# Performance work log

Hardware: AMD Instinct MI355X
Metric: run time of the kernel (lower is better)

## Reference

```python
import jax, jax.numpy as jnp
import numpy as np

H = 1024          # en_hidden_size
NUM_LAYERS = 3
NUM_CLASS = 60
IN_SIZE = 150
EPS = 1e-5


def _gru_dir(x, w_ih, w_hh, b_ih, b_hh):
    """Single-direction GRU run forward in time. x: [N,T,in] -> [N,T,H].
    PyTorch GRU cell math."""
    gi = jnp.einsum('nti,gi->ntg', x, w_ih) + b_ih  # [N,T,3H] input projections

    def step(h, gi_t):
        gh = h @ w_hh.T + b_hh
        i_r, i_z, i_n = jnp.split(gi_t, 3, axis=-1)
        h_r, h_z, h_n = jnp.split(gh, 3, axis=-1)
        r = jax.nn.sigmoid(i_r + h_r)
        z = jax.nn.sigmoid(i_z + h_z)
        n = jnp.tanh(i_n + r * h_n)
        h_new = (1.0 - z) * n + z * h
        return h_new, h_new

    h0 = jnp.zeros((x.shape[0], H), dtype=x.dtype)
    _, ys = jax.lax.scan(step, h0, jnp.swapaxes(gi, 0, 1))  # ys: [T,N,H]
    return jnp.swapaxes(ys, 0, 1)


def _bigru_forward(x, bn_gamma, bn_beta,
                   w_ih_0, w_hh_0, b_ih_0, b_hh_0,
                   w_ih_1, w_hh_1, b_ih_1, b_hh_1,
                   w_ih_2, w_hh_2, b_ih_2, b_hh_2,
                   fc_w, fc_b):
    # BatchNorm1d (train mode): stats over (N,T) per channel, biased variance.
    mean = jnp.mean(x, axis=(0, 1), keepdims=True)
    var = jnp.mean(jnp.square(x - mean), axis=(0, 1), keepdims=True)
    h_in = (x - mean) * jax.lax.rsqrt(var + EPS) * bn_gamma + bn_beta

    # NOTE: the original advances the bidirectional GRU one timestep at a time
    # while carrying the hidden state, so BOTH directions run forward in time.
    layer_params = [(w_ih_0, w_hh_0, b_ih_0, b_hh_0),
                    (w_ih_1, w_hh_1, b_ih_1, b_hh_1),
                    (w_ih_2, w_hh_2, b_ih_2, b_hh_2)]
    for (w_ih, w_hh, b_ih, b_hh) in layer_params:
        outs = [_gru_dir(h_in, w_ih[d], w_hh[d], b_ih[d], b_hh[d]) for d in range(2)]
        h_in = jnp.concatenate(outs, axis=-1)  # [N,T,2H]

    encoder_hidden = h_in                      # [N,T,2H]
    hidden = encoder_hidden[:, -1, :]          # seq_len == T for every sample
    out = hidden @ fc_w.T + fc_b               # [N, num_class]
    return out, encoder_hidden


def setup_inputs() -> dict:
    key = jax.random.key(0)
    ks = jax.random.split(key, 32)
    N, T = 256, 64
    s = 1.0 / np.sqrt(H)
    inp = {}
    inp['x'] = jax.random.normal(ks[0], (N, T, IN_SIZE), dtype=jnp.float32)
    inp['bn_gamma'] = jnp.ones((IN_SIZE,), jnp.float32)
    inp['bn_beta'] = jnp.zeros((IN_SIZE,), jnp.float32)
    in_sizes = [IN_SIZE, 2 * H, 2 * H]
    ki = 1
    for l in range(NUM_LAYERS):
        inp[f'w_ih_{l}'] = jax.random.uniform(ks[ki], (2, 3 * H, in_sizes[l]), jnp.float32, -s, s); ki += 1
        inp[f'w_hh_{l}'] = jax.random.uniform(ks[ki], (2, 3 * H, H), jnp.float32, -s, s); ki += 1
        inp[f'b_ih_{l}'] = jax.random.uniform(ks[ki], (2, 3 * H), jnp.float32, -s, s); ki += 1
        inp[f'b_hh_{l}'] = jax.random.uniform(ks[ki], (2, 3 * H), jnp.float32, -s, s); ki += 1
    inp['fc_w'] = jax.random.uniform(ks[ki], (NUM_CLASS, 2 * H), jnp.float32, -s, s); ki += 1
    inp['fc_b'] = jax.random.uniform(ks[ki], (NUM_CLASS,), jnp.float32, -s, s)
    return inp


def reference(x, bn_gamma, bn_beta,
              w_ih_0, w_hh_0, b_ih_0, b_hh_0,
              w_ih_1, w_hh_1, b_ih_1, b_hh_1,
              w_ih_2, w_hh_2, b_ih_2, b_hh_2,
              fc_w, fc_b):
    return _bigru_forward(x, bn_gamma, bn_beta,
                          w_ih_0, w_hh_0, b_ih_0, b_hh_0,
                          w_ih_1, w_hh_1, b_ih_1, b_hh_1,
                          w_ih_2, w_hh_2, b_ih_2, b_hh_2,
                          fc_w, fc_b)
```

## Files before the change

### kernel.cpp

```cpp
#include <hip/hip_runtime.h>
#include <hip/hip_bf16.h>
#include <hip/hip_fp16.h>
#include <math.h>

#define HH    1024
#define TT    64
#define NBAT  256
#define G3    3072
#define IN0   150
#define IN0P  160
#define NCLS  60
#define ENC_W 2048

typedef float  f32x4 __attribute__((ext_vector_type(4)));
typedef short  s16x8 __attribute__((ext_vector_type(8)));

#define GLOAD16(gsrc, ldst) \
  __builtin_amdgcn_global_load_lds((const __attribute__((address_space(1))) unsigned int*)(gsrc), \
                                   (__attribute__((address_space(3))) unsigned int*)(ldst), 16, 0, 0)

static __device__ inline short f2bf(float f) {
    __hip_bfloat16 h = __float2bfloat16(f);
    return *(short*)&h;
}

__global__ void bigru_bn_stats(const float* __restrict__ x,
                               float* __restrict__ mean, float* __restrict__ istd) {
    int f = blockIdx.x;
    int tid = threadIdx.x;
    double s = 0.0, s2 = 0.0;
    for (int i = tid; i < NBAT * TT; i += blockDim.x) {
        float v = x[(size_t)i * IN0 + f];
        s += v; s2 += (double)v * v;
    }
    __shared__ double sh[256], sh2[256];
    sh[tid] = s; sh2[tid] = s2;
    __syncthreads();
    for (int off = 128; off > 0; off >>= 1) {
        if (tid < off) { sh[tid] += sh[tid + off]; sh2[tid] += sh2[tid + off]; }
        __syncthreads();
    }
    if (tid == 0) {
        double m = sh[0] / (NBAT * TT);
        double var = sh2[0] / (NBAT * TT) - m * m;
        mean[f] = (float)m;
        istd[f] = (float)(1.0 / sqrt(var + 1e-5));
    }
}

__global__ void bigru_bn_apply_bf16(const float* __restrict__ x,
                                    const float* __restrict__ mean, const float* __restrict__ istd,
                                    const float* __restrict__ gamma, const float* __restrict__ beta,
                                    short* __restrict__ xn) {
    int idx = blockIdx.x * blockDim.x + threadIdx.x;
    if (idx >= NBAT * TT * IN0P) return;
    int f = idx % IN0P;
    int r = idx / IN0P;
    float v = 0.f;
    if (f < IN0) v = (x[(size_t)r * IN0 + f] - mean[f]) * istd[f] * gamma[f] + beta[f];
    xn[idx] = f2bf(v);
}

__global__ void bigru_cvt_wih0(const float* __restrict__ src, short* __restrict__ dst) {
    int idx = blockIdx.x * blockDim.x + threadIdx.x;
    if (idx >= 2 * G3 * IN0P) return;
    int f = idx % IN0P;
    int r = idx / IN0P;
    float v = (f < IN0) ? src[(size_t)r * IN0 + f] : 0.f;
    dst[idx] = f2bf(v);
}

__global__ void bigru_cvt4(const float* __restrict__ src, short* __restrict__ dst, int n4) {
    int i = blockIdx.x * blockDim.x + threadIdx.x;
    if (i >= n4) return;
    float4 v = ((const float4*)src)[i];
    short4 o;
    o.x = f2bf(v.x); o.y = f2bf(v.y); o.z = f2bf(v.z); o.w = f2bf(v.w);
    ((short4*)dst)[i] = o;
}

__global__ __launch_bounds__(256)
void bigru_gi_gemm(const short* __restrict__ Abase, int ldA, int K,
                   const short* __restrict__ W,
                   const float* __restrict__ b_ih,
                   __half* __restrict__ gi,
                   int t0, int Mchunk) {
    int d    = blockIdx.z;
    int col0 = blockIdx.x * 128;
    int row0 = blockIdx.y * 128;

    __shared__ short As[128][32];
    __shared__ short Bs[128][32];

    int tid  = threadIdx.x;
    int lane = tid & 63;
    int w    = tid >> 6;
    int wm   = w & 1, wn = w >> 1;

    f32x4 acc[4][4];
    #pragma unroll
    for (int i = 0; i < 4; ++i)
        #pragma unroll
        for (int j = 0; j < 4; ++j)
            acc[i][j] = (f32x4){0.f, 0.f, 0.f, 0.f};

    const short* Wd = W + (size_t)d * G3 * K;
    int sr = lane >> 2;
    int sc = (lane & 3) * 8;

    for (int k0 = 0; k0 < K; k0 += 32) {
        #pragma unroll
        for (int q = 0; q < 2; ++q) {
            int r  = w * 32 + q * 16 + sr;
            int gr = row0 + r;
            int tt = gr >> 8, n = gr & 255;
            const short* ga = Abase + (size_t)(n * TT + t0 + tt) * ldA + k0 + sc;
            GLOAD16(ga, &As[w * 32 + q * 16][0]);
            const short* gb = Wd + (size_t)(col0 + r) * K + k0 + sc;
            GLOAD16(gb, &Bs[w * 32 + q * 16][0]);
        }
        __syncthreads();

        int fr = lane & 15, fq = (lane >> 4) * 8;
        s16x8 a[4], b[4];
        #pragma unroll
        for (int i = 0; i < 4; ++i) a[i] = *(const s16x8*)&As[wm * 64 + i * 16 + fr][fq];
        #pragma unroll
        for (int j = 0; j < 4; ++j) b[j] = *(const s16x8*)&Bs[wn * 64 + j * 16 + fr][fq];
        #pragma unroll
        for (int i = 0; i < 4; ++i)
            #pragma unroll
            for (int j = 0; j < 4; ++j)
                acc[i][j] = __builtin_amdgcn_mfma_f32_16x16x32_bf16(a[i], b[j], acc[i][j], 0, 0, 0);
        __syncthreads();
    }

    int fr = lane & 15, quad = lane >> 4;
    #pragma unroll
    for (int j = 0; j < 4; ++j) {
        int c = col0 + wn * 64 + j * 16 + fr;
        float bias = b_ih[d * G3 + c];
        #pragma unroll
        for (int i = 0; i < 4; ++i) {
            #pragma unroll
            for (int reg = 0; reg < 4; ++reg) {
                int r = row0 + wm * 64 + i * 16 + quad * 4 + reg;
                gi[((size_t)d * Mchunk + r) * G3 + c] = __float2half(acc[i][j][reg] + bias);
            }
        }
    }
}

__global__ __launch_bounds__(256, 1)
void bigru_steps_fused(const short* __restrict__ w_hh,
                       const float* __restrict__ b_hh,
                       const __half* __restrict__ gi,
                       float* __restrict__ h,
                       short* __restrict__ hbf,
                       float* __restrict__ enc,
                       short* __restrict__ enc_bf,
                       unsigned int* __restrict__ bar,
                       int t0, int Tc, int Mchunk) {
    __shared__ short Ws[48 * 1024];
    __shared__ short As[4][4][1024];

    int b   = blockIdx.x;
    int d   = b & 1;
    int mt  = (b >> 1) & 1;
    int ct  = b >> 2;
    int grp = b & 3;

    int tid  = threadIdx.x;
    int lane = tid & 63;
    int w    = tid >> 6;
    int fr   = lane & 15;
    int quad = lane >> 4;
    int sw   = fr & 7;

    int j0 = ct * 16;
    int row_base = mt * 128 + w * 32;
    int jcol = j0 + fr;

    const short* Wd = w_hh + (size_t)d * G3 * HH;

    #pragma unroll
    for (int q = 0; q < 24; ++q) {
        int c  = w * 24 + q;
        int rr = c >> 1, kh = c & 1;
        int g  = rr >> 4, jc = rr & 15;
        const short* src = Wd + (size_t)(g * HH + j0 + jc) * HH
                         + (size_t)(kh * 64 + (lane ^ (rr & 7))) * 8;
        GLOAD16(src, &Ws[rr * 1024 + kh * 512]);
    }

    int l0 = lane & 1, l1 = (lane >> 1) & 1, l2 = (lane >> 2) & 1;
    int l3 = (lane >> 3) & 1, l4 = (lane >> 4) & 1, l5 = (lane >> 5) & 1;
    int arow = (l2 ^ l4) | (l3 << 1) | (l4 << 2) | (l5 << 3);
    int akb  = (l0 ^ l2 ^ l4) | ((l1 ^ l3) << 1);
    size_t a_src0 = (size_t)(row_base + arow) * HH + (size_t)akb * 8;
    size_t a_src1 = (size_t)(row_base + 16 + arow) * HH + (size_t)akb * 8;

    float hreg[2][4];
    #pragma unroll
    for (int hh = 0; hh < 2; ++hh)
        #pragma unroll
        for (int r = 0; r < 4; ++r) {
            int n = row_base + hh * 16 + quad * 4 + r;
            hreg[hh][r] = h[((size_t)d * NBAT + n) * HH + jcol];
        }
    float bhr = b_hh[d * G3 + jcol];
    float bhz = b_hh[d * G3 + HH + jcol];
    float bhn = b_hh[d * G3 + 2 * HH + jcol];

    __syncthreads();

    float gir[2][4], giz[2][4], gin[2][4];
    {
        size_t gb0 = ((size_t)d * Mchunk) * G3 + jcol;
        #pragma unroll
        for (int hh = 0; hh < 2; ++hh)
            #pragma unroll
            for (int r = 0; r < 4; ++r) {
                int n = row_base + hh * 16 + quad * 4 + r;
                size_t gg = gb0 + (size_t)n * G3;
                gir[hh][r] = __half2float(gi[gg]);
                giz[hh][r] = __half2float(gi[gg + HH]);
                gin[hh][r] = __half2float(gi[gg + 2 * HH]);
            }
    }

    for (int tt = 0; tt < Tc; ++tt) {
        int t = t0 + tt;
        const short* hb = hbf + ((size_t)((t & 1) * 2 + d)) * NBAT * HH;
        short*       ho = hbf + ((size_t)(((t + 1) & 1) * 2 + d)) * NBAT * HH;
        const short* asrc0 = hb + a_src0;
        const short* asrc1 = hb + a_src1;

        f32x4 acc[2][3];
        #pragma unroll
        for (int hh = 0; hh < 2; ++hh)
            #pragma unroll
            for (int g = 0; g < 3; ++g)
                acc[hh][g] = (f32x4){0.f, 0.f, 0.f, 0.f};

        #pragma unroll
        for (int c = 0; c < 3; ++c) {
            GLOAD16(asrc0 + c * 32, &As[w][c][0]);
            GLOAD16(asrc1 + c * 32, &As[w][c][512]);
        }

        int rd_off = (fr * 64 + quad * 16) ^ ((fr & 7) << 4);

        #pragma unroll
        for (int c = 0; c < 32; ++c) {
            if (c < 30)       asm volatile("s_waitcnt vmcnt(4)");
            else if (c == 30) asm volatile("s_waitcnt vmcnt(2)");
            else              asm volatile("s_waitcnt vmcnt(0)");
            __builtin_amdgcn_sched_barrier(0);
            const char* slot = (const char*)&As[w][c & 3][0];
            s16x8 a0 = *(const s16x8*)(slot + rd_off);
            s16x8 a1 = *(const s16x8*)(slot + 1024 + rd_off);
            int ks = c * 4 + quad;
            #pragma unroll
            for (int g = 0; g < 3; ++g) {
                s16x8 bg = *(const s16x8*)&Ws[(g * 16 + fr) * 1024 + ((ks ^ sw) << 3)];
                acc[0][g] = __builtin_amdgcn_mfma_f32_16x16x32_bf16(a0, bg, acc[0][g], 0, 0, 0);
                acc[1][g] = __builtin_amdgcn_mfma_f32_16x16x32_bf16(a1, bg, acc[1][g], 0, 0, 0);
            }
            __builtin_amdgcn_sched_barrier(0);
            if (c + 3 < 32) {
                GLOAD16(asrc0 + (c + 3) * 32, &As[w][(c + 3) & 3][0]);
                GLOAD16(asrc1 + (c + 3) * 32, &As[w][(c + 3) & 3][512]);
            }
        }

        #pragma unroll
        for (int hh = 0; hh < 2; ++hh) {
            #pragma unroll
            for (int r = 0; r < 4; ++r) {
                int n = row_base + hh * 16 + quad * 4 + r;
                float hrv = acc[hh][0][r] + bhr;
                float hzv = acc[hh][1][r] + bhz;
                float hnv = acc[hh][2][r] + bhn;
                float rg = 1.f / (1.f + __expf(-(gir[hh][r] + hrv)));
                float zg = 1.f / (1.f + __expf(-(giz[hh][r] + hzv)));
                float ng = tanhf(gin[hh][r] + rg * hnv);
                float hnew = (1.f - zg) * ng + zg * hreg[hh][r];
                hreg[hh][r] = hnew;
                ho[(size_t)n * HH + jcol] = f2bf(hnew);
                size_t eidx = ((size_t)n * TT + t) * ENC_W + (size_t)d * HH + jcol;
                if (enc_bf) enc_bf[eidx] = f2bf(hnew);
                if (enc)    enc[eidx]    = hnew;
            }
        }

        if (tt == Tc - 1) {
            #pragma unroll
            for (int hh = 0; hh < 2; ++hh)
                #pragma unroll
                for (int r = 0; r < 4; ++r) {
                    int n = row_base + hh * 16 + quad * 4 + r;
                    h[((size_t)d * NBAT + n) * HH + jcol] = hreg[hh][r];
                }
        } else {
            size_t gbn = ((size_t)d * Mchunk + (size_t)(tt + 1) * NBAT) * G3 + jcol;
            #pragma unroll
            for (int hh = 0; hh < 2; ++hh)
                #pragma unroll
                for (int r = 0; r < 4; ++r) {
                    int n = row_base + hh * 16 + quad * 4 + r;
                    size_t gg = gbn + (size_t)n * G3;
                    gir[hh][r] = __half2float(gi[gg]);
                    giz[hh][r] = __half2float(gi[gg + HH]);
                    gin[hh][r] = __half2float(gi[gg + 2 * HH]);
                }
            __syncthreads();
            if (w == 0) {
                unsigned int* fl = bar + (size_t)grp * 64 * 32;
                unsigned tgt = (unsigned)(tt + 1);
                if (lane == 0)
                    __hip_atomic_store(&fl[ct * 32], tgt,
                                       __ATOMIC_RELEASE, __HIP_MEMORY_SCOPE_AGENT);
                for (;;) {
                    unsigned v = __hip_atomic_load(&fl[lane * 32],
                                                   __ATOMIC_ACQUIRE, __HIP_MEMORY_SCOPE_AGENT);
                    if (__all(v >= tgt)) break;
                    __builtin_amdgcn_s_sleep(2);
                }
            }
            __syncthreads();
        }
    }
}

__global__ void bigru_fc(const float* __restrict__ enc, const float* __restrict__ fc_w,
                         const float* __restrict__ fc_b, float* __restrict__ out) {
    int n = blockIdx.x;
    int tid = threadIdx.x;
    __shared__ float hbuf[ENC_W];
    for (int k = tid; k < ENC_W; k += blockDim.x)
        hbuf[k] = enc[(size_t)n * TT * ENC_W + (size_t)(TT - 1) * ENC_W + k];
    __syncthreads();
    if (tid < NCLS) {
        float acc = fc_b[tid];
        for (int k = 0; k < ENC_W; ++k)
            acc += hbuf[k] * fc_w[(size_t)tid * ENC_W + k];
        out[(size_t)n * NCLS + tid] = acc;
    }
}

extern "C" void kernel_launch(void* const* d_in, const int* in_sizes, int n_in,
                              void* d_out, int out_size, void* d_ws, size_t ws_size,
                              hipStream_t stream) {
    const float* x        = (const float*)d_in[0];
    const float* bn_gamma = (const float*)d_in[1];
    const float* bn_beta  = (const float*)d_in[2];
    const float* w_ih[3]  = {(const float*)d_in[3], (const float*)d_in[7],  (const float*)d_in[11]};
    const float* w_hh[3]  = {(const float*)d_in[4], (const float*)d_in[8],  (const float*)d_in[12]};
    const float* b_ih[3]  = {(const float*)d_in[5], (const float*)d_in[9],  (const float*)d_in[13]};
    const float* b_hh[3]  = {(const float*)d_in[6], (const float*)d_in[10], (const float*)d_in[14]};
    const float* fc_w     = (const float*)d_in[15];
    const float* fc_b     = (const float*)d_in[16];

    float* out = (float*)d_out;
    float* enc = out + NBAT * NCLS;

    char* base = (char*)d_ws;
    size_t off = 0;
    auto alloc = [&](size_t bytes) {
        void* p = base + off;
        off += (bytes + 255) & ~(size_t)255;
        return p;
    };
    float* mean      = (float*)alloc(IN0 * 4);
    float* istd      = (float*)alloc(IN0 * 4);
    short* xn_bf     = (short*)alloc((size_t)NBAT * TT * IN0P * 2);
    short* wih0_bf   = (short*)alloc((size_t)2 * G3 * IN0P * 2);
    short* wih_bf    = (short*)alloc((size_t)2 * G3 * ENC_W * 2);
    short* whh_bf    = (short*)alloc((size_t)2 * G3 * HH * 2);
    float* h         = (float*)alloc((size_t)2 * NBAT * HH * 4);
    short* hbf       = (short*)alloc((size_t)2 * 2 * NBAT * HH * 2);
    short* enc_bf    = (short*)alloc((size_t)NBAT * TT * ENC_W * 2);
    unsigned int* bar = (unsigned int*)alloc((size_t)4 * 64 * 32 * sizeof(unsigned int));
    size_t fixed = off;

    int Tc = 1;
    for (int cand : {16, 8, 4, 2, 1}) {
        size_t gi_bytes = (size_t)2 * NBAT * cand * G3 * 2;
        if (fixed + gi_bytes + 1024 <= ws_size) { Tc = cand; break; }
    }
    __half* gi = (__half*)alloc((size_t)2 * NBAT * Tc * G3 * 2);
    int Mchunk = NBAT * Tc;

    bigru_bn_stats<<<IN0, 256, 0, stream>>>(x, mean, istd);
    bigru_bn_apply_bf16<<<(NBAT * TT * IN0P + 255) / 256, 256, 0, stream>>>(
        x, mean, istd, bn_gamma, bn_beta, xn_bf);

    bigru_cvt_wih0<<<(2 * G3 * IN0P + 255) / 256, 256, 0, stream>>>(w_ih[0], wih0_bf);

    for (int l = 0; l < 3; ++l) {
        if (l > 0) {
            int n4 = (2 * G3 * ENC_W) / 4;
            bigru_cvt4<<<(n4 + 255) / 256, 256, 0, stream>>>(w_ih[l], wih_bf, n4);
        }
        {
            int n4 = (2 * G3 * HH) / 4;
            bigru_cvt4<<<(n4 + 255) / 256, 256, 0, stream>>>(w_hh[l], whh_bf, n4);
        }
        hipMemsetAsync(h, 0, (size_t)2 * NBAT * HH * 4, stream);
        hipMemsetAsync(hbf, 0, (size_t)2 * 2 * NBAT * HH * 2, stream);

        const short* Abase = (l == 0) ? xn_bf : enc_bf;
        int ldA = (l == 0) ? IN0P : ENC_W;
        int K   = (l == 0) ? IN0P : ENC_W;
        const short* W = (l == 0) ? wih0_bf : wih_bf;

        for (int t0 = 0; t0 < TT; t0 += Tc) {
            bigru_gi_gemm<<<dim3(G3 / 128, Mchunk / 128, 2), 256, 0, stream>>>(
                Abase, ldA, K, W, b_ih[l], gi, t0, Mchunk);

            hipMemsetAsync(bar, 0, (size_t)4 * 64 * 32 * sizeof(unsigned int), stream);

            const short* whh_c   = whh_bf;
            const float* bhh_c   = b_hh[l];
            const __half* gi_c   = gi;
            float*       h_c     = h;
            short*       hbf_c   = hbf;
            float*       enc_c   = (l == 2) ? enc : nullptr;
            short*       encbf_c = (l == 2) ? nullptr : enc_bf;
            unsigned int* bar_c  = bar;
            int a_t0 = t0, a_tc = Tc, a_mc = Mchunk;
            void* kargs[] = { &whh_c, &bhh_c, &gi_c, &h_c, &hbf_c,
                              &enc_c, &encbf_c, &bar_c, &a_t0, &a_tc, &a_mc };
            hipLaunchCooperativeKernel((const void*)bigru_steps_fused,
                                       dim3(256), dim3(256), kargs, 0, stream);
        }
    }

    bigru_fc<<<NBAT, 256, 0, stream>>>(enc, fc_w, fc_b, out);
}
```

Measured before the change: 4.879 ms.

## Replace persistent cooperative step kernel with per-timestep kernel launches

Removes the cooperative persistent kernel that looped over timesteps with atomic flag barriers between block groups. Each timestep now launches a separate kernel, relying on kernel boundaries for synchronization. This avoids the spin-wait barrier and the barrier memset. In exchange, each launch reloads its recurrent weight slice into LDS and the hidden state from global memory, and adds per-launch overhead.

```diff
diff --git a/kernel.cpp b/kernel.cpp
--- a/kernel.cpp
+++ b/kernel.cpp
@@ -152,15 +152,15 @@
 }
 
 __global__ __launch_bounds__(256, 1)
-void bigru_steps_fused(const short* __restrict__ w_hh,
-                       const float* __restrict__ b_hh,
-                       const __half* __restrict__ gi,
-                       float* __restrict__ h,
-                       short* __restrict__ hbf,
-                       float* __restrict__ enc,
-                       short* __restrict__ enc_bf,
-                       unsigned int* __restrict__ bar,
-                       int t0, int Tc, int Mchunk) {
+void bigru_step(const short* __restrict__ w_hh,
+                const float* __restrict__ b_hh,
+                const __half* __restrict__ gi,
+                float* __restrict__ h,
+                const short* __restrict__ hbf_in,
+                short* __restrict__ hbf_out,
+                float* __restrict__ enc,
+                short* __restrict__ enc_bf,
+                int t, int ttl, int Mchunk) {
     __shared__ short Ws[48 * 1024];
     __shared__ short As[4][4][1024];
 
@@ -168,7 +168,6 @@
     int d   = b & 1;
     int mt  = (b >> 1) & 1;
     int ct  = b >> 2;
-    int grp = b & 3;
 
     int tid  = threadIdx.x;
     int lane = tid & 63;
@@ -197,138 +196,87 @@
     int l3 = (lane >> 3) & 1, l4 = (lane >> 4) & 1, l5 = (lane >> 5) & 1;
     int arow = (l2 ^ l4) | (l3 << 1) | (l4 << 2) | (l5 << 3);
     int akb  = (l0 ^ l2 ^ l4) | ((l1 ^ l3) << 1);
-    size_t a_src0 = (size_t)(row_base + arow) * HH + (size_t)akb * 8;
-    size_t a_src1 = (size_t)(row_base + 16 + arow) * HH + (size_t)akb * 8;
-
-    float hreg[2][4];
-    #pragma unroll
-    for (int hh = 0; hh < 2; ++hh)
-        #pragma unroll
-        for (int r = 0; r < 4; ++r) {
-            int n = row_base + hh * 16 + quad * 4 + r;
-            hreg[hh][r] = h[((size_t)d * NBAT + n) * HH + jcol];
-        }
-    float bhr = b_hh[d * G3 + jcol];
-    float bhz = b_hh[d * G3 + HH + jcol];
-    float bhn = b_hh[d * G3 + 2 * HH + jcol];
-
-    __syncthreads();
-
-    float gir[2][4], giz[2][4], gin[2][4];
+    const short* hb = hbf_in + (size_t)d * NBAT * HH;
+    const short* asrc0 = hb + (size_t)(row_base + arow) * HH + (size_t)akb * 8;
+    const short* asrc1 = hb + (size_t)(row_base + 16 + arow) * HH + (size_t)akb * 8;
+
+    float gir[2][4], giz[2][4], gin[2][4], hreg[2][4];
     {
-        size_t gb0 = ((size_t)d * Mchunk) * G3 + jcol;
+        size_t gb = ((size_t)d * Mchunk + (size_t)ttl * NBAT) * G3 + jcol;
         #pragma unroll
         for (int hh = 0; hh < 2; ++hh)
             #pragma unroll
             for (int r = 0; r < 4; ++r) {
                 int n = row_base + hh * 16 + quad * 4 + r;
-                size_t gg = gb0 + (size_t)n * G3;
+                size_t gg = gb + (size_t)n * G3;
                 gir[hh][r] = __half2float(gi[gg]);
                 giz[hh][r] = __half2float(gi[gg + HH]);
                 gin[hh][r] = __half2float(gi[gg + 2 * HH]);
+                hreg[hh][r] = h[((size_t)d * NBAT + n) * HH + jcol];
             }
     }
-
-    for (int tt = 0; tt < Tc; ++tt) {
-        int t = t0 + tt;
-        const short* hb = hbf + ((size_t)((t & 1) * 2 + d)) * NBAT * HH;
-        short*       ho = hbf + ((size_t)(((t + 1) & 1) * 2 + d)) * NBAT * HH;
-        const short* asrc0 = hb + a_src0;
-        const short* asrc1 = hb + a_src1;
-
-        f32x4 acc[2][3];
-        #pragma unroll
-        for (int hh = 0; hh < 2; ++hh)
-            #pragma unroll
-            for (int g = 0; g < 3; ++g)
-                acc[hh][g] = (f32x4){0.f, 0.f, 0.f, 0.f};
-
-        #pragma unroll
-        for (int c = 0; c < 3; ++c) {
-            GLOAD16(asrc0 + c * 32, &As[w][c][0]);
-            GLOAD16(asrc1 + c * 32, &As[w][c][512]);
-        }
-
-        int rd_off = (fr * 64 + quad * 16) ^ ((fr & 7) << 4);
-
-        #pragma unroll
-        for (int c = 0; c < 32; ++c) {
-            if (c < 30)       asm volatile("s_waitcnt vmcnt(4)");
-            else if (c == 30) asm volatile("s_waitcnt vmcnt(2)");
-            else              asm volatile("s_waitcnt vmcnt(0)");
-            __builtin_amdgcn_sched_barrier(0);
-            const char* slot = (const char*)&As[w][c & 3][0];
-            s16x8 a0 = *(const s16x8*)(slot + rd_off);
-            s16x8 a1 = *(const s16x8*)(slot + 1024 + rd_off);
-            int ks = c * 4 + quad;
-            #pragma unroll
-            for (int g = 0; g < 3; ++g) {
-                s16x8 bg = *(const s16x8*)&Ws[(g * 16 + fr) * 1024 + ((ks ^ sw) << 3)];
-                acc[0][g] = __builtin_amdgcn_mfma_f32_16x16x32_bf16(a0, bg, acc[0][g], 0, 0, 0);
-                acc[1][g] = __builtin_amdgcn_mfma_f32_16x16x32_bf16(a1, bg, acc[1][g], 0, 0, 0);
-            }
-            __builtin_amdgcn_sched_barrier(0);
-            if (c + 3 < 32) {
-                GLOAD16(asrc0 + (c + 3) * 32, &As[w][(c + 3) & 3][0]);
-                GLOAD16(asrc1 + (c + 3) * 32, &As[w][(c + 3) & 3][512]);
-            }
-        }
-
-        #pragma unroll
-        for (int hh = 0; hh < 2; ++hh) {
-            #pragma unroll
-            for (int r = 0; r < 4; ++r) {
-                int n = row_base + hh * 16 + quad * 4 + r;
-                float hrv = acc[hh][0][r] + bhr;
-                float hzv = acc[hh][1][r] + bhz;
-                float hnv = acc[hh][2][r] + bhn;
-                float rg = 1.f / (1.f + __expf(-(gir[hh][r] + hrv)));
-                float zg = 1.f / (1.f + __expf(-(giz[hh][r] + hzv)));
-                float ng = tanhf(gin[hh][r] + rg * hnv);
-                float hnew = (1.f - zg) * ng + zg * hreg[hh][r];
-                hreg[hh][r] = hnew;
-                ho[(size_t)n * HH + jcol] = f2bf(hnew);
-                size_t eidx = ((size_t)n * TT + t) * ENC_W + (size_t)d * HH + jcol;
-                if (enc_bf) enc_bf[eidx] = f2bf(hnew);
-                if (enc)    enc[eidx]    = hnew;
-            }
-        }
-
-        if (tt == Tc - 1) {
-            #pragma unroll
-            for (int hh = 0; hh < 2; ++hh)
-                #pragma unroll
-                for (int r = 0; r < 4; ++r) {
-                    int n = row_base + hh * 16 + quad * 4 + r;
-                    h[((size_t)d * NBAT + n) * HH + jcol] = hreg[hh][r];
-                }
-        } else {
-            size_t gbn = ((size_t)d * Mchunk + (size_t)(tt + 1) * NBAT) * G3 + jcol;
-            #pragma unroll
-            for (int hh = 0; hh < 2; ++hh)
-                #pragma unroll
-                for (int r = 0; r < 4; ++r) {
-                    int n = row_base + hh * 16 + quad * 4 + r;
-                    size_t gg = gbn + (size_t)n * G3;
-                    gir[hh][r] = __half2float(gi[gg]);
-                    giz[hh][r] = __half2float(gi[gg + HH]);
-                    gin[hh][r] = __half2float(gi[gg + 2 * HH]);
-                }
-            __syncthreads();
-            if (w == 0) {
-                unsigned int* fl = bar + (size_t)grp * 64 * 32;
-                unsigned tgt = (unsigned)(tt + 1);
-                if (lane == 0)
-                    __hip_atomic_store(&fl[ct * 32], tgt,
-                                       __ATOMIC_RELEASE, __HIP_MEMORY_SCOPE_AGENT);
-                for (;;) {
-                    unsigned v = __hip_atomic_load(&fl[lane * 32],
-                                                   __ATOMIC_ACQUIRE, __HIP_MEMORY_SCOPE_AGENT);
-                    if (__all(v >= tgt)) break;
-                    __builtin_amdgcn_s_sleep(2);
-                }
-            }
-            __syncthreads();
+    float bhr = b_hh[d * G3 + jcol];
+    float bhz = b_hh[d * G3 + HH + jcol];
+    float bhn = b_hh[d * G3 + 2 * HH + jcol];
+
+    __syncthreads();
+
+    f32x4 acc[2][3];
+    #pragma unroll
+    for (int hh = 0; hh < 2; ++hh)
+        #pragma unroll
+        for (int g = 0; g < 3; ++g)
+            acc[hh][g] = (f32x4){0.f, 0.f, 0.f, 0.f};
+
+    #pragma unroll
+    for (int c = 0; c < 3; ++c) {
+        GLOAD16(asrc0 + c * 32, &As[w][c][0]);
+        GLOAD16(asrc1 + c * 32, &As[w][c][512]);
+    }
+
+    int rd_off = (fr * 64 + quad * 16) ^ ((fr & 7) << 4);
+
+    #pragma unroll
+    for (int c = 0; c < 32; ++c) {
+        if (c < 30)       asm volatile("s_waitcnt vmcnt(4)");
+        else if (c == 30) asm volatile("s_waitcnt vmcnt(2)");
+        else              asm volatile("s_waitcnt vmcnt(0)");
+        __builtin_amdgcn_sched_barrier(0);
+        const char* slot = (const char*)&As[w][c & 3][0];
+        s16x8 a0 = *(const s16x8*)(slot + rd_off);
+        s16x8 a1 = *(const s16x8*)(slot + 1024 + rd_off);
+        int ks = c * 4 + quad;
+        #pragma unroll
+        for (int g = 0; g < 3; ++g) {
+            s16x8 bg = *(const s16x8*)&Ws[(g * 16 + fr) * 1024 + ((ks ^ sw) << 3)];
+            acc[0][g] = __builtin_amdgcn_mfma_f32_16x16x32_bf16(a0, bg, acc[0][g], 0, 0, 0);
+            acc[1][g] = __builtin_amdgcn_mfma_f32_16x16x32_bf16(a1, bg, acc[1][g], 0, 0, 0);
+        }
+        __builtin_amdgcn_sched_barrier(0);
+        if (c + 3 < 32) {
+            GLOAD16(asrc0 + (c + 3) * 32, &As[w][(c + 3) & 3][0]);
+            GLOAD16(asrc1 + (c + 3) * 32, &As[w][(c + 3) & 3][512]);
+        }
+    }
+
+    short* ho = hbf_out + (size_t)d * NBAT * HH;
+    #pragma unroll
+    for (int hh = 0; hh < 2; ++hh) {
+        #pragma unroll
+        for (int r = 0; r < 4; ++r) {
+            int n = row_base + hh * 16 + quad * 4 + r;
+            float hrv = acc[hh][0][r] + bhr;
+            float hzv = acc[hh][1][r] + bhz;
+            float hnv = acc[hh][2][r] + bhn;
+            float rg = 1.f / (1.f + __expf(-(gir[hh][r] + hrv)));
+            float zg = 1.f / (1.f + __expf(-(giz[hh][r] + hzv)));
+            float ng = tanhf(gin[hh][r] + rg * hnv);
+            float hnew = (1.f - zg) * ng + zg * hreg[hh][r];
+            h[((size_t)d * NBAT + n) * HH + jcol] = hnew;
+            ho[(size_t)n * HH + jcol] = f2bf(hnew);
+            size_t eidx = ((size_t)n * TT + t) * ENC_W + (size_t)d * HH + jcol;
+            if (enc_bf) enc_bf[eidx] = f2bf(hnew);
+            if (enc)    enc[eidx]    = hnew;
         }
     }
 }
@@ -381,7 +329,6 @@
     float* h         = (float*)alloc((size_t)2 * NBAT * HH * 4);
     short* hbf       = (short*)alloc((size_t)2 * 2 * NBAT * HH * 2);
     short* enc_bf    = (short*)alloc((size_t)NBAT * TT * ENC_W * 2);
-    unsigned int* bar = (unsigned int*)alloc((size_t)4 * 64 * 32 * sizeof(unsigned int));
     size_t fixed = off;
 
     int Tc = 1;
@@ -414,26 +361,21 @@
         int ldA = (l == 0) ? IN0P : ENC_W;
         int K   = (l == 0) ? IN0P : ENC_W;
         const short* W = (l == 0) ? wih0_bf : wih_bf;
+        float* enc_out   = (l == 2) ? enc : nullptr;
+        short* encbf_out = (l == 2) ? nullptr : enc_bf;
 
         for (int t0 = 0; t0 < TT; t0 += Tc) {
             bigru_gi_gemm<<<dim3(G3 / 128, Mchunk / 128, 2), 256, 0, stream>>>(
                 Abase, ldA, K, W, b_ih[l], gi, t0, Mchunk);
 
-            hipMemsetAsync(bar, 0, (size_t)4 * 64 * 32 * sizeof(unsigned int), stream);
-
-            const short* whh_c   = whh_bf;
-            const float* bhh_c   = b_hh[l];
-            const __half* gi_c   = gi;
-            float*       h_c     = h;
-            short*       hbf_c   = hbf;
-            float*       enc_c   = (l == 2) ? enc : nullptr;
-            short*       encbf_c = (l == 2) ? nullptr : enc_bf;
-            unsigned int* bar_c  = bar;
-            int a_t0 = t0, a_tc = Tc, a_mc = Mchunk;
-            void* kargs[] = { &whh_c, &bhh_c, &gi_c, &h_c, &hbf_c,
-                              &enc_c, &encbf_c, &bar_c, &a_t0, &a_tc, &a_mc };
-            hipLaunchCooperativeKernel((const void*)bigru_steps_fused,
-                                       dim3(256), dim3(256), kargs, 0, stream);
+            for (int tt = 0; tt < Tc; ++tt) {
+                int t = t0 + tt;
+                const short* hin = hbf + (size_t)(t & 1) * 2 * NBAT * HH;
+                short*       hout = hbf + (size_t)((t + 1) & 1) * 2 * NBAT * HH;
+                bigru_step<<<dim3(256), 256, 0, stream>>>(
+                    whh_bf, b_hh[l], gi, h, hin, hout,
+                    enc_out, encbf_out, t, tt, Mchunk);
+            }
         }
     }
 
```

Result: faster. 4.301 ms (-11.8%).
